# Performance work log

Measured on AMD Instinct MI355X. Metric: run time of the kernel, lower is better.

## Reference

```python
import jax, jax.numpy as jnp
import numpy as np

HIDDEN = 1024
HEADS = 16
HEAD_DIM = HIDDEN // HEADS  # 64
LOCAL = (128, 128)
ROPE_MAX_POS = LOCAL[0] + LOCAL[1]  # 256 (local attention branch)
ROPE_BASE = 10000.0


def make_rope_cache(max_len, dim, base):
    positions = jnp.arange(max_len, dtype=jnp.float32)
    theta = 1.0 / base ** (jnp.arange(0, dim, 2, dtype=jnp.float32) / dim)
    angles = jnp.einsum('i,j->ij', positions, theta)
    return jnp.stack([jnp.cos(angles), jnp.sin(angles)], axis=-1)  # (max_len, dim//2, 2)


def apply_rope(x, cache):
    # x: (B, S, H, D); cache: (max_pos, D//2, 2)
    S = x.shape[1]
    pos = jnp.arange(S) % cache.shape[0]
    rc = cache[pos][None, :, None, :, :]  # (1, S, 1, D//2, 2)
    xr = x.reshape(*x.shape[:-1], -1, 2)
    x0, x1 = xr[..., 0], xr[..., 1]
    c, s = rc[..., 0], rc[..., 1]
    out = jnp.stack([x0 * c - x1 * s, x1 * c + x0 * s], axis=-1)
    return out.reshape(x.shape)


def sliding_window_mask(S, window, dtype):
    rel = jnp.arange(S)[:, None] - jnp.arange(S)[None, :]
    inside = (rel >= -window[0]) & (rel <= window[1])
    return jnp.where(inside, jnp.zeros((), dtype), -jnp.inf)[None, None]  # (1,1,S,S)


def setup_inputs() -> dict:
    key = jax.random.key(0)
    k1, k2, k3, k4, k5 = jax.random.split(key, 5)
    B, S = 2, 2048
    hidden_states = jax.random.normal(k1, (B, S, HIDDEN), dtype=jnp.float32)
    Wqkv_kernel = jax.random.normal(k2, (HIDDEN, 3 * HIDDEN), dtype=jnp.float32) / np.sqrt(HIDDEN)
    Wqkv_bias = jnp.zeros((3 * HIDDEN,), dtype=jnp.float32)
    Wo_kernel = jax.random.normal(k3, (HIDDEN, HIDDEN), dtype=jnp.float32) / np.sqrt(HIDDEN)
    Wo_bias = jnp.zeros((HIDDEN,), dtype=jnp.float32)
    rope_cache = make_rope_cache(ROPE_MAX_POS, HEAD_DIM, ROPE_BASE)
    return {
        'hidden_states': hidden_states,
        'Wqkv_kernel': Wqkv_kernel,
        'Wqkv_bias': Wqkv_bias,
        'Wo_kernel': Wo_kernel,
        'Wo_bias': Wo_bias,
        'rope_cache': rope_cache,
    }


def reference(hidden_states, Wqkv_kernel, Wqkv_bias, Wo_kernel, Wo_bias, rope_cache):
    B, S, _ = hidden_states.shape
    qkv = hidden_states @ Wqkv_kernel + Wqkv_bias  # (B,S,3*HIDDEN)
    qkv = qkv.reshape(B, S, 3, HEADS, HEAD_DIM)
    q = qkv[:, :, 0]  # (B,S,H,D)
    k = qkv[:, :, 1]
    v = qkv[:, :, 2]
    q = apply_rope(q, rope_cache)
    k = apply_rope(k, rope_cache)
    # to (B,H,S,D)
    q = jnp.transpose(q, (0, 2, 1, 3))
    k = jnp.transpose(k, (0, 2, 1, 3))
    v = jnp.transpose(v, (0, 2, 1, 3))
    scale = jnp.sqrt(jnp.float32(HEAD_DIM))
    scores = jnp.einsum('bhqd,bhkd->bhqk', q, k) / scale
    mask = sliding_window_mask(S, LOCAL, scores.dtype)
    probs = jax.nn.softmax(scores + mask, axis=-1)
    out = jnp.einsum('bhqk,bhkd->bqhd', probs, v).reshape(B, S, HIDDEN)
    out = out @ Wo_kernel + Wo_bias
    return out
```

## Files before the change

kernel.cpp:

```cpp
#include <hip/hip_runtime.h>
#include <hip/hip_bf16.h>

typedef __bf16 bf16x8 __attribute__((ext_vector_type(8)));
typedef __bf16 bf16x4 __attribute__((ext_vector_type(4)));
typedef float f32x4 __attribute__((ext_vector_type(4)));

#define SLEN 2048
#define NHEADS 16
#define HDIM 64

__global__ __launch_bounds__(256) void cast_f32_bf16(const float* __restrict__ in,
                                                     __bf16* __restrict__ out, int n4) {
    int i = blockIdx.x * 256 + threadIdx.x;
    if (i < n4) {
        float4 v = reinterpret_cast<const float4*>(in)[i];
        bf16x4 o = { (__bf16)v.x, (__bf16)v.y, (__bf16)v.z, (__bf16)v.w };
        reinterpret_cast<bf16x4*>(out)[i] = o;
    }
}

__global__ __launch_bounds__(256) void transpose_cast(const float* __restrict__ W,
                                                      __bf16* __restrict__ Wt,
                                                      int K, int N) {
    __shared__ float tile[32][33];
    int n0 = blockIdx.x * 32, k0 = blockIdx.y * 32;
    int tx = threadIdx.x, ty = threadIdx.y;
    #pragma unroll
    for (int i = ty; i < 32; i += 8)
        tile[i][tx] = W[(size_t)(k0 + i) * N + n0 + tx];
    __syncthreads();
    #pragma unroll
    for (int i = ty; i < 32; i += 8)
        Wt[(size_t)(n0 + i) * K + k0 + tx] = (__bf16)tile[tx][i];
}

template <int TN>
__global__ __launch_bounds__(256) void gemm_bt(const __bf16* __restrict__ A,
                                               const __bf16* __restrict__ Bt,
                                               const float* __restrict__ bias,
                                               const float* __restrict__ rope,
                                               float* __restrict__ Cf,
                                               __bf16* __restrict__ Cq,
                                               __bf16* __restrict__ Ck,
                                               __bf16* __restrict__ Cv,
                                               int M, int N, int K, int epi) {
    constexpr int JN = TN / 32;
    __shared__ __align__(16) __bf16 As[128 * 32];
    __shared__ __align__(16) __bf16 Bs[TN * 32];

    int nb = N / TN;
    int bx = blockIdx.x % nb;
    int by = blockIdx.x / nb;
    int row0 = by * 128, col0 = bx * TN;

    int tid = threadIdx.x;
    int wave = tid >> 6, lane = tid & 63;
    int quad = lane >> 4, lrow = lane & 15;
    int wm = wave >> 1, wn = wave & 1;

    int r1 = tid >> 2;
    int kk = (tid & 3) * 8;
    int kg = kk ^ (((r1 >> 1) & 3) * 8);
    const __bf16* Ap = A + (size_t)(row0 + r1) * K + kg;
    const __bf16* Bp = Bt + (size_t)(col0 + r1) * K + kg;

    f32x4 acc[4][JN];
    f32x4 zero = {0.f, 0.f, 0.f, 0.f};
    #pragma unroll
    for (int i = 0; i < 4; i++)
        #pragma unroll
        for (int j = 0; j < JN; j++) acc[i][j] = zero;

    int sA = (quad ^ ((lrow >> 1) & 3)) * 8;

    for (int k0 = 0; k0 < K; k0 += 32) {
        bf16x8 a0 = *reinterpret_cast<const bf16x8*>(Ap + k0);
        bf16x8 a1 = *reinterpret_cast<const bf16x8*>(Ap + (size_t)64 * K + k0);
        bf16x8 b0 = *reinterpret_cast<const bf16x8*>(Bp + k0);
        bf16x8 b1;
        if (TN == 128) b1 = *reinterpret_cast<const bf16x8*>(Bp + (size_t)64 * K + k0);
        __syncthreads();
        *reinterpret_cast<bf16x8*>(&As[r1 * 32 + kk]) = a0;
        *reinterpret_cast<bf16x8*>(&As[(r1 + 64) * 32 + kk]) = a1;
        *reinterpret_cast<bf16x8*>(&Bs[r1 * 32 + kk]) = b0;
        if (TN == 128) *reinterpret_cast<bf16x8*>(&Bs[(r1 + 64) * 32 + kk]) = b1;
        __syncthreads();

        bf16x8 af[4], bfr[JN];
        #pragma unroll
        for (int i = 0; i < 4; i++)
            af[i] = *reinterpret_cast<const bf16x8*>(&As[(wm * 64 + i * 16 + lrow) * 32 + sA]);
        #pragma unroll
        for (int j = 0; j < JN; j++)
            bfr[j] = *reinterpret_cast<const bf16x8*>(&Bs[(wn * (TN / 2) + j * 16 + lrow) * 32 + sA]);
        #pragma unroll
        for (int i = 0; i < 4; i++)
            #pragma unroll
            for (int j = 0; j < JN; j++)
                acc[i][j] = __builtin_amdgcn_mfma_f32_16x16x32_bf16(af[i], bfr[j], acc[i][j], 0, 0, 0);
    }

    int part = col0 >> 10;
    bool do_rope = (epi == 1) && (part < 2);
    #pragma unroll
    for (int i = 0; i < 4; i++) {
        int rowb = row0 + wm * 64 + i * 16 + quad * 4;
        #pragma unroll
        for (int j = 0; j < JN; j++) {
            int col = col0 + wn * (TN / 2) + j * 16 + lrow;
            float bsv = bias[col];
            int d = col & 63;
            #pragma unroll
            for (int r = 0; r < 4; r++) {
                int row = rowb + r;
                float v = acc[i][j][r] + bsv;
                if (do_rope) {
                    int pos = row & 255;
                    int p = d >> 1;
                    float c  = rope[(pos * 32 + p) * 2];
                    float sn = rope[(pos * 32 + p) * 2 + 1];
                    float other = __shfl_xor(v, 1, 64);
                    v = (d & 1) ? fmaf(v, c, other * sn) : fmaf(v, c, -other * sn);
                }
                if (epi == 0) {
                    Cf[(size_t)row * N + col] = v;
                } else {
                    int h = (col >> 6) & 15;
                    int b = row >> 11;
                    int s = row & 2047;
                    __bf16* dst = (part == 0) ? Cq : ((part == 1) ? Ck : Cv);
                    dst[((size_t)(b * NHEADS + h) * SLEN + s) * HDIM + d] = (__bf16)v;
                }
            }
        }
    }
}

__global__ __launch_bounds__(256) void attn_kernel(const __bf16* __restrict__ Q,
                                                   const __bf16* __restrict__ K,
                                                   const __bf16* __restrict__ V,
                                                   __bf16* __restrict__ O) {
    __shared__ __align__(16) __bf16 Vt[64][328];
    __shared__ __align__(16) __bf16 Pl[4][16][40];

    int qt = blockIdx.x & 31;
    int bh = blockIdx.x >> 5;
    int q0 = qt * 64;
    int kbase0 = q0 - 128;
    const __bf16* Qbh = Q + (size_t)bh * SLEN * HDIM;
    const __bf16* Kbh = K + (size_t)bh * SLEN * HDIM;
    const __bf16* Vbh = V + (size_t)bh * SLEN * HDIM;

    int tid = threadIdx.x;
    int wave = tid >> 6, lane = tid & 63;
    int quad = lane >> 4, lrow = lane & 15;
    int wq0 = q0 + wave * 16;

    {
        int dchunk = wave * 16;
        #pragma unroll
        for (int k = 0; k < 5; k++) {
            int off = k * 64 + lane;
            int krow = kbase0 + off;
            krow = min(max(krow, 0), SLEN - 1);
            const __bf16* vp = Vbh + (size_t)krow * HDIM + dchunk;
            bf16x8 v0 = *reinterpret_cast<const bf16x8*>(vp);
            bf16x8 v1 = *reinterpret_cast<const bf16x8*>(vp + 8);
            #pragma unroll
            for (int i = 0; i < 8; i++) {
                Vt[dchunk + i][off] = v0[i];
                Vt[dchunk + 8 + i][off] = v1[i];
            }
        }
    }

    bf16x8 qb0 = *reinterpret_cast<const bf16x8*>(Qbh + (size_t)(wq0 + lrow) * HDIM + quad * 8);
    bf16x8 qb1 = *reinterpret_cast<const bf16x8*>(Qbh + (size_t)(wq0 + lrow) * HDIM + 32 + quad * 8);

    __syncthreads();

    f32x4 zero = {0.f, 0.f, 0.f, 0.f};
    f32x4 acc[4], acc_l = zero;
    #pragma unroll
    for (int t = 0; t < 4; t++) acc[t] = zero;

    bf16x8 ones = { (__bf16)1.f, (__bf16)1.f, (__bf16)1.f, (__bf16)1.f,
                    (__bf16)1.f, (__bf16)1.f, (__bf16)1.f, (__bf16)1.f };

    int cbeg = wave >> 1;
    if (q0 < 128) { int e = (128 - q0) >> 5; if (e > cbeg) cbeg = e; }
    int cend = (16 * wave + 271) >> 5;
    { int e = (2175 - q0) >> 5; if (e < cend) cend = e; }

    for (int c = cbeg; c <= cend; c++) {
        int kb = kbase0 + c * 32;
        int loc = c * 32;

        f32x4 st[2];
        #pragma unroll
        for (int sub = 0; sub < 2; sub++) {
            int kr = kb + sub * 16 + lrow;
            int krc = min(max(kr, 0), SLEN - 1);
            const __bf16* kp = Kbh + (size_t)krc * HDIM;
            bf16x8 ka0 = *reinterpret_cast<const bf16x8*>(kp + quad * 8);
            bf16x8 ka1 = *reinterpret_cast<const bf16x8*>(kp + 32 + quad * 8);
            st[sub] = __builtin_amdgcn_mfma_f32_16x16x32_bf16(ka0, qb0, zero, 0, 0, 0);
            st[sub] = __builtin_amdgcn_mfma_f32_16x16x32_bf16(ka1, qb1, st[sub], 0, 0, 0);
        }

        int q = wq0 + lrow;
        #pragma unroll
        for (int sub = 0; sub < 2; sub++) {
            bf16x4 pk;
            #pragma unroll
            for (int r = 0; r < 4; r++) {
                int key = kb + sub * 16 + quad * 4 + r;
                int rel = key - q;
                bool valid = (rel >= -128) && (rel <= 128) && (key >= 0) && (key < SLEN);
                float p = valid ? __expf(st[sub][r] * 0.125f) : 0.0f;
                pk[r] = (__bf16)p;
            }
            *reinterpret_cast<bf16x4*>(&Pl[wave][lrow][sub * 16 + quad * 4]) = pk;
        }
        asm volatile("s_waitcnt lgkmcnt(0)" ::: "memory");

        bf16x8 bp = *reinterpret_cast<const bf16x8*>(&Pl[wave][lrow][quad * 8]);
        acc_l = __builtin_amdgcn_mfma_f32_16x16x32_bf16(ones, bp, acc_l, 0, 0, 0);
        #pragma unroll
        for (int t = 0; t < 4; t++) {
            bf16x8 va = *reinterpret_cast<const bf16x8*>(&Vt[t * 16 + lrow][loc + quad * 8]);
            acc[t] = __builtin_amdgcn_mfma_f32_16x16x32_bf16(va, bp, acc[t], 0, 0, 0);
        }
    }

    float inv = 1.0f / acc_l[0];
    int b = bh >> 4, h = bh & 15;
    int q = wq0 + lrow;
    size_t base = ((size_t)b * SLEN + q) * 1024 + h * HDIM;
    #pragma unroll
    for (int t = 0; t < 4; t++) {
        bf16x4 o;
        #pragma unroll
        for (int r = 0; r < 4; r++) o[r] = (__bf16)(acc[t][r] * inv);
        *reinterpret_cast<bf16x4*>(&O[base + t * 16 + quad * 4]) = o;
    }
}

extern "C" void kernel_launch(void* const* d_in, const int* in_sizes, int n_in,
                              void* d_out, int out_size, void* d_ws, size_t ws_size,
                              hipStream_t stream) {
    const float* hidden = (const float*)d_in[0];
    const float* Wqkv   = (const float*)d_in[1];
    const float* bqkv   = (const float*)d_in[2];
    const float* Wo     = (const float*)d_in[3];
    const float* bo     = (const float*)d_in[4];
    const float* rope   = (const float*)d_in[5];
    float* out = (float*)d_out;

    char* ws = (char*)d_ws;
    __bf16* A1  = (__bf16*)(ws);
    __bf16* Wt  = (__bf16*)(ws + 8388608);
    __bf16* Wot = (__bf16*)(ws + 14680064);
    __bf16* Qb  = (__bf16*)(ws + 16777216);
    __bf16* Kb  = (__bf16*)(ws + 25165824);
    __bf16* Vb  = (__bf16*)(ws + 33554432);
    __bf16* AO  = (__bf16*)(ws + 41943040);

    cast_f32_bf16<<<4096, 256, 0, stream>>>(hidden, A1, 1048576);
    transpose_cast<<<dim3(96, 32), dim3(32, 8), 0, stream>>>(Wqkv, Wt, 1024, 3072);
    transpose_cast<<<dim3(32, 32), dim3(32, 8), 0, stream>>>(Wo, Wot, 1024, 1024);

    gemm_bt<128><<<32 * 24, 256, 0, stream>>>(A1, Wt, bqkv, rope, nullptr, Qb, Kb, Vb,
                                              4096, 3072, 1024, 1);
    attn_kernel<<<1024, 256, 0, stream>>>(Qb, Kb, Vb, AO);
    gemm_bt<64><<<32 * 16, 256, 0, stream>>>(AO, Wot, bo, rope, out, nullptr, nullptr, nullptr,
                                             4096, 1024, 1024, 0);
}
```

Before: 201.0 us.

## Merge prep kernels, pad GEMM LDS tiles, move RoPE into attention loads

```diff
diff --git a/kernel.cpp b/kernel.cpp
--- a/kernel.cpp
+++ b/kernel.cpp
@@ -9,44 +9,47 @@
 #define NHEADS 16
 #define HDIM 64
 
-__global__ __launch_bounds__(256) void cast_f32_bf16(const float* __restrict__ in,
-                                                     __bf16* __restrict__ out, int n4) {
-    int i = blockIdx.x * 256 + threadIdx.x;
-    if (i < n4) {
-        float4 v = reinterpret_cast<const float4*>(in)[i];
+__global__ __launch_bounds__(256) void prep(const float* __restrict__ hidden,
+                                            const float* __restrict__ Wqkv,
+                                            const float* __restrict__ Wo,
+                                            __bf16* __restrict__ A1,
+                                            __bf16* __restrict__ Wt,
+                                            __bf16* __restrict__ Wot) {
+    int b = blockIdx.x;
+    if (b < 4096) {
+        int i = b * 256 + threadIdx.x;
+        float4 v = reinterpret_cast<const float4*>(hidden)[i];
         bf16x4 o = { (__bf16)v.x, (__bf16)v.y, (__bf16)v.z, (__bf16)v.w };
-        reinterpret_cast<bf16x4*>(out)[i] = o;
-    }
-}
-
-__global__ __launch_bounds__(256) void transpose_cast(const float* __restrict__ W,
-                                                      __bf16* __restrict__ Wt,
-                                                      int K, int N) {
-    __shared__ float tile[32][33];
-    int n0 = blockIdx.x * 32, k0 = blockIdx.y * 32;
-    int tx = threadIdx.x, ty = threadIdx.y;
-    #pragma unroll
-    for (int i = ty; i < 32; i += 8)
-        tile[i][tx] = W[(size_t)(k0 + i) * N + n0 + tx];
-    __syncthreads();
-    #pragma unroll
-    for (int i = ty; i < 32; i += 8)
-        Wt[(size_t)(n0 + i) * K + k0 + tx] = (__bf16)tile[tx][i];
+        reinterpret_cast<bf16x4*>(A1)[i] = o;
+    } else {
+        __shared__ float tile[32][33];
+        const float* W; __bf16* Dst; int N, bx, by;
+        if (b < 7168) { int bb = b - 4096; W = Wqkv; Dst = Wt;  N = 3072; bx = bb % 96; by = bb / 96; }
+        else          { int bb = b - 7168; W = Wo;   Dst = Wot; N = 1024; bx = bb % 32; by = bb / 32; }
+        int tx = threadIdx.x & 31, ty = threadIdx.x >> 5;
+        int n0 = bx * 32, k0 = by * 32;
+        #pragma unroll
+        for (int i = ty; i < 32; i += 8)
+            tile[i][tx] = W[(size_t)(k0 + i) * N + n0 + tx];
+        __syncthreads();
+        #pragma unroll
+        for (int i = ty; i < 32; i += 8)
+            Dst[(size_t)(n0 + i) * 1024 + k0 + tx] = (__bf16)tile[tx][i];
+    }
 }
 
 template <int TN>
 __global__ __launch_bounds__(256) void gemm_bt(const __bf16* __restrict__ A,
                                                const __bf16* __restrict__ Bt,
                                                const float* __restrict__ bias,
-                                               const float* __restrict__ rope,
                                                float* __restrict__ Cf,
                                                __bf16* __restrict__ Cq,
                                                __bf16* __restrict__ Ck,
                                                __bf16* __restrict__ Cv,
                                                int M, int N, int K, int epi) {
     constexpr int JN = TN / 32;
-    __shared__ __align__(16) __bf16 As[128 * 32];
-    __shared__ __align__(16) __bf16 Bs[TN * 32];
+    __shared__ __align__(16) __bf16 As[128 * 40];
+    __shared__ __align__(16) __bf16 Bs[TN * 40];
 
     int nb = N / TN;
     int bx = blockIdx.x % nb;
@@ -60,9 +63,8 @@
 
     int r1 = tid >> 2;
     int kk = (tid & 3) * 8;
-    int kg = kk ^ (((r1 >> 1) & 3) * 8);
-    const __bf16* Ap = A + (size_t)(row0 + r1) * K + kg;
-    const __bf16* Bp = Bt + (size_t)(col0 + r1) * K + kg;
+    const __bf16* Aptr = A + (size_t)(row0 + r1) * K + kk;
+    const __bf16* Bptr = Bt + (size_t)(col0 + r1) * K + kk;
 
     f32x4 acc[4][JN];
     f32x4 zero = {0.f, 0.f, 0.f, 0.f};
@@ -71,28 +73,26 @@
         #pragma unroll
         for (int j = 0; j < JN; j++) acc[i][j] = zero;
 
-    int sA = (quad ^ ((lrow >> 1) & 3)) * 8;
-
     for (int k0 = 0; k0 < K; k0 += 32) {
-        bf16x8 a0 = *reinterpret_cast<const bf16x8*>(Ap + k0);
-        bf16x8 a1 = *reinterpret_cast<const bf16x8*>(Ap + (size_t)64 * K + k0);
-        bf16x8 b0 = *reinterpret_cast<const bf16x8*>(Bp + k0);
+        bf16x8 a0 = *reinterpret_cast<const bf16x8*>(Aptr + k0);
+        bf16x8 a1 = *reinterpret_cast<const bf16x8*>(Aptr + (size_t)64 * K + k0);
+        bf16x8 b0 = *reinterpret_cast<const bf16x8*>(Bptr + k0);
         bf16x8 b1;
-        if (TN == 128) b1 = *reinterpret_cast<const bf16x8*>(Bp + (size_t)64 * K + k0);
+        if (TN == 128) b1 = *reinterpret_cast<const bf16x8*>(Bptr + (size_t)64 * K + k0);
         __syncthreads();
-        *reinterpret_cast<bf16x8*>(&As[r1 * 32 + kk]) = a0;
-        *reinterpret_cast<bf16x8*>(&As[(r1 + 64) * 32 + kk]) = a1;
-        *reinterpret_cast<bf16x8*>(&Bs[r1 * 32 + kk]) = b0;
-        if (TN == 128) *reinterpret_cast<bf16x8*>(&Bs[(r1 + 64) * 32 + kk]) = b1;
+        *reinterpret_cast<bf16x8*>(&As[r1 * 40 + kk]) = a0;
+        *reinterpret_cast<bf16x8*>(&As[(r1 + 64) * 40 + kk]) = a1;
+        *reinterpret_cast<bf16x8*>(&Bs[r1 * 40 + kk]) = b0;
+        if (TN == 128) *reinterpret_cast<bf16x8*>(&Bs[(r1 + 64) * 40 + kk]) = b1;
         __syncthreads();
 
         bf16x8 af[4], bfr[JN];
         #pragma unroll
         for (int i = 0; i < 4; i++)
-            af[i] = *reinterpret_cast<const bf16x8*>(&As[(wm * 64 + i * 16 + lrow) * 32 + sA]);
+            af[i] = *reinterpret_cast<const bf16x8*>(&As[(wm * 64 + i * 16 + lrow) * 40 + quad * 8]);
         #pragma unroll
         for (int j = 0; j < JN; j++)
-            bfr[j] = *reinterpret_cast<const bf16x8*>(&Bs[(wn * (TN / 2) + j * 16 + lrow) * 32 + sA]);
+            bfr[j] = *reinterpret_cast<const bf16x8*>(&Bs[(wn * (TN / 2) + j * 16 + lrow) * 40 + quad * 8]);
         #pragma unroll
         for (int i = 0; i < 4; i++)
             #pragma unroll
@@ -101,7 +101,6 @@
     }
 
     int part = col0 >> 10;
-    bool do_rope = (epi == 1) && (part < 2);
     #pragma unroll
     for (int i = 0; i < 4; i++) {
         int rowb = row0 + wm * 64 + i * 16 + quad * 4;
@@ -109,23 +108,15 @@
         for (int j = 0; j < JN; j++) {
             int col = col0 + wn * (TN / 2) + j * 16 + lrow;
             float bsv = bias[col];
-            int d = col & 63;
             #pragma unroll
             for (int r = 0; r < 4; r++) {
                 int row = rowb + r;
                 float v = acc[i][j][r] + bsv;
-                if (do_rope) {
-                    int pos = row & 255;
-                    int p = d >> 1;
-                    float c  = rope[(pos * 32 + p) * 2];
-                    float sn = rope[(pos * 32 + p) * 2 + 1];
-                    float other = __shfl_xor(v, 1, 64);
-                    v = (d & 1) ? fmaf(v, c, other * sn) : fmaf(v, c, -other * sn);
-                }
                 if (epi == 0) {
                     Cf[(size_t)row * N + col] = v;
                 } else {
                     int h = (col >> 6) & 15;
+                    int d = col & 63;
                     int b = row >> 11;
                     int s = row & 2047;
                     __bf16* dst = (part == 0) ? Cq : ((part == 1) ? Ck : Cv);
@@ -136,9 +127,24 @@
     }
 }
 
+__device__ __forceinline__ bf16x8 rope8(bf16x8 v, f32x4 a, f32x4 b) {
+    bf16x8 o;
+    float e, od;
+    e = (float)v[0]; od = (float)v[1];
+    o[0] = (__bf16)(e * a[0] - od * a[1]); o[1] = (__bf16)(od * a[0] + e * a[1]);
+    e = (float)v[2]; od = (float)v[3];
+    o[2] = (__bf16)(e * a[2] - od * a[3]); o[3] = (__bf16)(od * a[2] + e * a[3]);
+    e = (float)v[4]; od = (float)v[5];
+    o[4] = (__bf16)(e * b[0] - od * b[1]); o[5] = (__bf16)(od * b[0] + e * b[1]);
+    e = (float)v[6]; od = (float)v[7];
+    o[6] = (__bf16)(e * b[2] - od * b[3]); o[7] = (__bf16)(od * b[2] + e * b[3]);
+    return o;
+}
+
 __global__ __launch_bounds__(256) void attn_kernel(const __bf16* __restrict__ Q,
                                                    const __bf16* __restrict__ K,
                                                    const __bf16* __restrict__ V,
+                                                   const float* __restrict__ rope,
                                                    __bf16* __restrict__ O) {
     __shared__ __align__(16) __bf16 Vt[64][328];
     __shared__ __align__(16) __bf16 Pl[4][16][40];
@@ -174,8 +180,16 @@
         }
     }
 
-    bf16x8 qb0 = *reinterpret_cast<const bf16x8*>(Qbh + (size_t)(wq0 + lrow) * HDIM + quad * 8);
-    bf16x8 qb1 = *reinterpret_cast<const bf16x8*>(Qbh + (size_t)(wq0 + lrow) * HDIM + 32 + quad * 8);
+    int posq = (wq0 + lrow) & 255;
+    const float* rq = rope + (size_t)posq * 64;
+    f32x4 qc0a = *reinterpret_cast<const f32x4*>(rq + quad * 8);
+    f32x4 qc0b = *reinterpret_cast<const f32x4*>(rq + quad * 8 + 4);
+    f32x4 qc1a = *reinterpret_cast<const f32x4*>(rq + 32 + quad * 8);
+    f32x4 qc1b = *reinterpret_cast<const f32x4*>(rq + 32 + quad * 8 + 4);
+    bf16x8 qb0 = rope8(*reinterpret_cast<const bf16x8*>(Qbh + (size_t)(wq0 + lrow) * HDIM + quad * 8),
+                       qc0a, qc0b);
+    bf16x8 qb1 = rope8(*reinterpret_cast<const bf16x8*>(Qbh + (size_t)(wq0 + lrow) * HDIM + 32 + quad * 8),
+                       qc1a, qc1b);
 
     __syncthreads();
 
@@ -202,8 +216,13 @@
             int kr = kb + sub * 16 + lrow;
             int krc = min(max(kr, 0), SLEN - 1);
             const __bf16* kp = Kbh + (size_t)krc * HDIM;
-            bf16x8 ka0 = *reinterpret_cast<const bf16x8*>(kp + quad * 8);
-            bf16x8 ka1 = *reinterpret_cast<const bf16x8*>(kp + 32 + quad * 8);
+            const float* rk = rope + (size_t)(krc & 255) * 64;
+            f32x4 kc0a = *reinterpret_cast<const f32x4*>(rk + quad * 8);
+            f32x4 kc0b = *reinterpret_cast<const f32x4*>(rk + quad * 8 + 4);
+            f32x4 kc1a = *reinterpret_cast<const f32x4*>(rk + 32 + quad * 8);
+            f32x4 kc1b = *reinterpret_cast<const f32x4*>(rk + 32 + quad * 8 + 4);
+            bf16x8 ka0 = rope8(*reinterpret_cast<const bf16x8*>(kp + quad * 8), kc0a, kc0b);
+            bf16x8 ka1 = rope8(*reinterpret_cast<const bf16x8*>(kp + 32 + quad * 8), kc1a, kc1b);
             st[sub] = __builtin_amdgcn_mfma_f32_16x16x32_bf16(ka0, qb0, zero, 0, 0, 0);
             st[sub] = __builtin_amdgcn_mfma_f32_16x16x32_bf16(ka1, qb1, st[sub], 0, 0, 0);
         }
@@ -266,13 +285,11 @@
     __bf16* Vb  = (__bf16*)(ws + 33554432);
     __bf16* AO  = (__bf16*)(ws + 41943040);
 
-    cast_f32_bf16<<<4096, 256, 0, stream>>>(hidden, A1, 1048576);
-    transpose_cast<<<dim3(96, 32), dim3(32, 8), 0, stream>>>(Wqkv, Wt, 1024, 3072);
-    transpose_cast<<<dim3(32, 32), dim3(32, 8), 0, stream>>>(Wo, Wot, 1024, 1024);
-
-    gemm_bt<128><<<32 * 24, 256, 0, stream>>>(A1, Wt, bqkv, rope, nullptr, Qb, Kb, Vb,
+    prep<<<8192, 256, 0, stream>>>(hidden, Wqkv, Wo, A1, Wt, Wot);
+
+    gemm_bt<128><<<32 * 24, 256, 0, stream>>>(A1, Wt, bqkv, nullptr, Qb, Kb, Vb,
                                               4096, 3072, 1024, 1);
-    attn_kernel<<<1024, 256, 0, stream>>>(Qb, Kb, Vb, AO);
-    gemm_bt<64><<<32 * 16, 256, 0, stream>>>(AO, Wot, bo, rope, out, nullptr, nullptr, nullptr,
+    attn_kernel<<<1024, 256, 0, stream>>>(Qb, Kb, Vb, rope, AO);
+    gemm_bt<64><<<32 * 16, 256, 0, stream>>>(AO, Wot, bo, out, nullptr, nullptr, nullptr,
                                              4096, 1024, 1024, 0);
 }
```

After: 211.6 us. 5.2% more time.
